# Kernel optimization log

Measured on AMD Instinct MI355X. Metric: run time of the kernel, lower is better.

The kernel has to match this reference:

```python
import jax, jax.numpy as jnp
import numpy as np
from jax import lax

B, T_CAP, V, E, D = 64, 32, 32000, 1024, 1024  # embed_dim == encoder_dim required by the module


def _lstm_cell(x, h, c, W_ih, W_hh, b_ih, b_hh):
    # gates: [B, 4D]; PyTorch LSTMCell gate order: i, f, g, o
    gates = x @ W_ih.T + b_ih + h @ W_hh.T + b_hh
    i, f, g, o = jnp.split(gates, 4, axis=-1)
    c_new = jax.nn.sigmoid(f) * c + jax.nn.sigmoid(i) * jnp.tanh(g)
    h_new = jax.nn.sigmoid(o) * jnp.tanh(c_new)
    return h_new, c_new


def setup_inputs() -> dict:
    key = jax.random.key(0)
    ks = jax.random.split(key, 9)
    encoder_out = jax.random.normal(ks[0], (B, E), jnp.float32)
    encoded_captions = jax.random.randint(ks[1], (B, T_CAP), 0, V, dtype=jnp.int64)
    caption_lengths = jax.random.randint(ks[2], (B, 1), 2, T_CAP + 1, dtype=jnp.int64)
    caption_lengths = caption_lengths.at[0, 0].set(T_CAP)  # ensure max decode len = T_CAP-1 (static)
    s = 1.0 / np.sqrt(D).astype(np.float32)
    embedding = jax.random.normal(ks[3], (V, E), jnp.float32)
    W_ih = jax.random.uniform(ks[4], (4 * D, E), jnp.float32, -s, s)
    W_hh = jax.random.uniform(ks[5], (4 * D, D), jnp.float32, -s, s)
    b_ih = jax.random.uniform(ks[6], (4 * D,), jnp.float32, -s, s)
    b_hh = jax.random.uniform(ks[7], (4 * D,), jnp.float32, -s, s)
    fc_W = jax.random.uniform(ks[8], (V, D), jnp.float32, -0.1, 0.1)  # reset_parameters
    fc_b = jnp.zeros((V,), jnp.float32)
    return {"encoder_out": encoder_out, "encoded_captions": encoded_captions,
            "caption_lengths": caption_lengths, "embedding": embedding,
            "W_ih": W_ih, "W_hh": W_hh, "b_ih": b_ih, "b_hh": b_hh,
            "fc_W": fc_W, "fc_b": fc_b}


def reference(encoder_out, encoded_captions, caption_lengths, embedding,
              W_ih, W_hh, b_ih, b_hh, fc_W, fc_b):
    lengths = caption_lengths[:, 0]
    sort_ind = jnp.argsort(-lengths)  # descending, stable (matches torch sort semantics)
    lengths = lengths[sort_ind]
    enc = encoder_out[sort_ind]                       # [B, E]
    caps = encoded_captions[sort_ind]                 # [B, T]
    emb = embedding[caps]                             # [B, T, E]
    decode_lengths = lengths - 1                      # [B]
    t_dec = emb.shape[1] - 1                          # static = T_CAP - 1

    zeros = jnp.zeros((enc.shape[0], D), enc.dtype)
    h, c = _lstm_cell(enc, zeros, zeros, W_ih, W_hh, b_ih, b_hh)  # warm-up step with encoder_out

    # masked update is equivalent to the torch :batch_size_t slicing because
    # lengths are sorted descending -> the active prefix only shrinks over t.
    masks = jnp.arange(t_dec)[:, None] < decode_lengths[None, :]  # [T-1, B]
    xs = jnp.swapaxes(emb[:, :t_dec], 0, 1)                       # [T-1, B, E]

    def step(carry, inp):
        h, c = carry
        x_t, m = inp
        hn, cn = _lstm_cell(x_t, h, c, W_ih, W_hh, b_ih, b_hh)
        m2 = m[:, None]
        h = jnp.where(m2, hn, h)
        c = jnp.where(m2, cn, c)
        # dropout in eval mode == identity
        preds = (h @ fc_W.T + fc_b) * m2.astype(h.dtype)  # inactive rows stay 0
        return (h, c), preds

    (_, _), preds = lax.scan(step, (h, c), (xs, masks))
    predictions = jnp.swapaxes(preds, 0, 1)  # [B, T-1, V]
    return predictions, decode_lengths, sort_ind
```

## Files before the change

kernel.cpp:

```cpp
#include <hip/hip_runtime.h>
#include <cstddef>
#include <cstdint>

#define PRED_N 63488000

typedef unsigned short u16;
typedef unsigned long long u64;
typedef __attribute__((ext_vector_type(8))) unsigned short us8;
typedef __attribute__((ext_vector_type(4))) float f32x4;
typedef __attribute__((ext_vector_type(8))) __bf16 bf16x8;

__device__ __forceinline__ float bf2f(u16 h){
  unsigned u = ((unsigned)h) << 16;
  return __builtin_bit_cast(float, u);
}
__device__ __forceinline__ u16 f2bf(float f){
  unsigned u = __builtin_bit_cast(unsigned, f);
  u += 0x7FFFu + ((u >> 16) & 1u);
  return (u16)(u >> 16);
}
__device__ __forceinline__ float sigf(float x){ return 1.f/(1.f + __expf(-x)); }
__device__ __forceinline__ float tanhf_(float x){ return 1.f - 2.f/(__expf(2.f*x) + 1.f); }

__device__ __forceinline__ f32x4 mfma16(us8 a, us8 b, f32x4 c){
  return __builtin_amdgcn_mfma_f32_16x16x32_bf16(
      __builtin_bit_cast(bf16x8, a), __builtin_bit_cast(bf16x8, b), c, 0, 0, 0);
}
__device__ __forceinline__ u64 pack4bf(const float* h){
  return (u64)f2bf(h[0]) | ((u64)f2bf(h[1]) << 16)
       | ((u64)f2bf(h[2]) << 32) | ((u64)f2bf(h[3]) << 48);
}
__device__ __forceinline__ us8 pack8(float4 a, float4 b){
  us8 r;
  r[0]=f2bf(a.x); r[1]=f2bf(a.y); r[2]=f2bf(a.z); r[3]=f2bf(a.w);
  r[4]=f2bf(b.x); r[5]=f2bf(b.y); r[6]=f2bf(b.z); r[7]=f2bf(b.w);
  return r;
}
__device__ __forceinline__ float ldf(const void* p, int f32, int i){
  return f32 ? ((const float*)p)[i] : bf2f(((const u16*)p)[i]);
}
__device__ __forceinline__ int ldi(const int* p, int i64, int i){
  return i64 ? p[2*i] : p[i];
}
__device__ __forceinline__ void stH(u16* p, u64 v){
  __hip_atomic_store((u64*)p, v, __ATOMIC_RELAXED, __HIP_MEMORY_SCOPE_AGENT);
}
__device__ __forceinline__ us8 ldH8(const u16* p){
  union { u64 q[2]; us8 v; } u;
  u.q[0] = __hip_atomic_load((const u64*)p,       __ATOMIC_RELAXED, __HIP_MEMORY_SCOPE_AGENT);
  u.q[1] = __hip_atomic_load((const u64*)(p + 4), __ATOMIC_RELAXED, __HIP_MEMORY_SCOPE_AGENT);
  return u.v;
}

__global__ void k_detect(const unsigned* __restrict__ embw, const int* __restrict__ lenw,
                         int* __restrict__ flags){
  if(threadIdx.x == 0){
    int hits = 0;
    for(int i = 0; i < 16; ++i){
      unsigned w = embw[i];
      int elo = (w >> 7) & 0xFF, ehi = (w >> 23) & 0xFF;
      hits += (elo >= 112 && elo <= 133) && (ehi >= 112 && ehi <= 133);
    }
    flags[0] = (hits >= 12) ? 0 : 1;
    int orv = 0;
    for(int i = 0; i < 4; ++i) orv |= lenw[2*i + 1];
    flags[1] = (orv == 0) ? 1 : 0;
    __hip_atomic_store((unsigned*)(flags + 48), 0u, __ATOMIC_RELAXED, __HIP_MEMORY_SCOPE_AGENT);
  }
}

__global__ void k_setup(const int* __restrict__ lens, int* __restrict__ wsI,
                        const int* __restrict__ flags, void* __restrict__ out){
  const int i = threadIdx.x;
  const int f32 = flags[0], i64 = flags[1];
  const int li = ldi(lens, i64, i);
  int rank = 0;
  for(int j = 0; j < 64; ++j){
    const int lj = ldi(lens, i64, j);
    rank += (lj > li) || (lj == li && j < i);
  }
  wsI[rank]      = i;
  wsI[64 + rank] = li - 1;
  if(f32){
    ((float*)out)[PRED_N + rank]      = (float)(li - 1);
    ((float*)out)[PRED_N + 64 + rank] = (float)i;
  } else {
    ((u16*)out)[PRED_N + rank]      = f2bf((float)(li - 1));
    ((u16*)out)[PRED_N + 64 + rank] = f2bf((float)i);
  }
}

__global__ void __launch_bounds__(256) k_conv16(const void* __restrict__ W,
    const int* __restrict__ flags, u16* __restrict__ dst, int n8){
  if(!flags[0]) return;
  const int stride = gridDim.x * 256;
  for(int i = blockIdx.x * 256 + threadIdx.x; i < n8; i += stride){
    const float4* s = (const float4*)W + 2 * (size_t)i;
    ((us8*)dst)[i] = pack8(s[0], s[1]);
  }
}

__global__ void __launch_bounds__(256) k_gather(const void* __restrict__ enc,
    const int* __restrict__ caps, const void* __restrict__ emb,
    const int* __restrict__ wsI, const int* __restrict__ flags, u16* __restrict__ X){
  const int r = blockIdx.x, t = r >> 6, b = r & 63;
  const int f32 = flags[0], i64 = flags[1];
  const int sb = wsI[b];
  const size_t rowoff = (t == 0) ? (size_t)sb * 1024
                                 : (size_t)ldi(caps, i64, sb * 32 + (t - 1)) * 1024;
  const void* base = (t == 0) ? enc : emb;
  u16* dst = X + (size_t)r * 1024;
  if(f32){
    const float4* src = (const float4*)((const float*)base + rowoff);
    float4 v = src[threadIdx.x];
    u64 w = (u64)f2bf(v.x) | ((u64)f2bf(v.y) << 16)
          | ((u64)f2bf(v.z) << 32) | ((u64)f2bf(v.w) << 48);
    ((u64*)dst)[threadIdx.x] = w;
  } else {
    const uint2* src = (const uint2*)((const u16*)base + rowoff);
    ((uint2*)dst)[threadIdx.x] = src[threadIdx.x];
  }
}

__device__ __forceinline__ void gemm_main(const u16* __restrict__ A, const void* __restrict__ Bv,
    int bF32, int arowmax, u16* As, u16* Bs, f32x4 (&acc)[4][4]){
  const int tid = threadIdx.x, wave = tid >> 6, lane = tid & 63;
  const int mq = (wave >> 1) * 64, nq = (wave & 1) * 64;
  const int l15 = lane & 15, lq = lane >> 4;
  const int r0 = lane >> 2, c0 = (lane & 3) * 8;
  const int sww = ((r0 & 7) << 3);
  const int swr = ((l15 & 7) << 3);
  const u16* Bb = (const u16*)Bv; const float* Bf = (const float*)Bv;
  for(int k0 = 0; k0 < 1024; k0 += 32){
    us8 av[2], bv[2];
#pragma unroll
    for(int c2 = 0; c2 < 2; ++c2){
      const int chunk = wave * 2 + c2;
      int ar = chunk * 16 + r0; if(ar > arowmax) ar = arowmax;
      av[c2] = *(const us8*)(A + (size_t)ar * 1024 + k0 + c0);
      const size_t bo = (size_t)(chunk * 16 + r0) * 1024 + k0 + c0;
      if(bF32){
        const float* p = Bf + bo;
        bv[c2] = pack8(*(const float4*)p, *(const float4*)(p + 4));
      } else {
        bv[c2] = *(const us8*)(Bb + bo);
      }
    }
    __syncthreads();
#pragma unroll
    for(int c2 = 0; c2 < 2; ++c2){
      const int chunk = wave * 2 + c2;
      *(us8*)&As[(chunk * 512 + r0 * 32 + c0) ^ sww] = av[c2];
      *(us8*)&Bs[(chunk * 512 + r0 * 32 + c0) ^ sww] = bv[c2];
    }
    __syncthreads();
    us8 af[4], bfv[4];
#pragma unroll
    for(int i = 0; i < 4; ++i){
      af[i]  = *(const us8*)&As[((mq + i * 16 + l15) * 32 + lq * 8) ^ swr];
      bfv[i] = *(const us8*)&Bs[((nq + i * 16 + l15) * 32 + lq * 8) ^ swr];
    }
#pragma unroll
    for(int i = 0; i < 4; ++i)
#pragma unroll
      for(int j = 0; j < 4; ++j)
        acc[i][j] = mfma16(af[i], bfv[j], acc[i][j]);
  }
}

__global__ void __launch_bounds__(256) k_gemm_gates(const u16* __restrict__ X,
    const void* __restrict__ Wih, const u16* __restrict__ Wih16c,
    const void* __restrict__ bih, const void* __restrict__ bhh,
    const int* __restrict__ flags, float* __restrict__ gatesx){
  __shared__ u16 As[4096], Bs[4096];
  const int tid = threadIdx.x, wave = tid >> 6, lane = tid & 63;
  const int bm = blockIdx.x, bn = blockIdx.y;
  const int mq = (wave >> 1) * 64, nq = (wave & 1) * 64;
  const int l15 = lane & 15, lq = lane >> 4;
  const int f32 = flags[0];
  const u16* Wb = f32 ? Wih16c : (const u16*)Wih;
  f32x4 acc[4][4] = {};
  gemm_main(X + (size_t)bm * 128 * 1024, Wb + (size_t)bn * 128 * 1024, 0, 127, As, Bs, acc);
  const int rowb = bm * 128 + mq, colb = bn * 128 + nq;
#pragma unroll
  for(int j = 0; j < 4; ++j){
    const int col = colb + j * 16 + l15;
    const float bias = ldf(bih, f32, col) + ldf(bhh, f32, col);
#pragma unroll
    for(int i = 0; i < 4; ++i)
#pragma unroll
      for(int v = 0; v < 4; ++v){
        const int row = rowb + i * 16 + lq * 4 + v;
        gatesx[(size_t)row * 4096 + col] = acc[i][j][v] + bias;
      }
  }
}

__device__ __forceinline__ void gbar(unsigned* bar, unsigned tgt, int tid){
  __syncthreads();
  if(tid == 0){
    __hip_atomic_fetch_add(bar, 1u, __ATOMIC_RELAXED, __HIP_MEMORY_SCOPE_AGENT);
    while(__hip_atomic_load(bar, __ATOMIC_RELAXED, __HIP_MEMORY_SCOPE_AGENT) < tgt)
      __builtin_amdgcn_s_sleep(2);
  }
  __syncthreads();
  asm volatile("" ::: "memory");
}

__global__ void __launch_bounds__(256, 1) k_rnn5(const void* __restrict__ Whh,
    const u16* __restrict__ Whh16c, const float* __restrict__ gatesx,
    const int* __restrict__ wsI, const int* __restrict__ flags,
    u16* __restrict__ Hbuf, unsigned* __restrict__ bar){
  __shared__ __align__(16) float red[4096];
  __shared__ __align__(16) float hl[256];
  const int tid = threadIdx.x, wave = tid >> 6, lane = tid & 63, blk = blockIdx.x;
  const int l15 = lane & 15, lq = lane >> 4;
  const int m = tid >> 2, dr = tid & 3;
  const int dim = blk * 4 + dr;
  const int dl = wsI[64 + m];
  const u16* W = flags[0] ? Whh16c : (const u16*)Whh;

  float c1, h1;
  {
    const float* gx0 = gatesx + (size_t)m * 4096 + dim;
    const float iv = gx0[0], gv = gx0[2048], ov = gx0[3072];
    c1 = sigf(iv) * tanhf_(gv);
    h1 = sigf(ov) * tanhf_(c1);
  }
  hl[m * 4 + dr] = h1;
  const int brow = (l15 >> 2) * 1024 + blk * 4 + (l15 & 3);
  us8 breg[8];
  {
    const u16* Bp = W + (size_t)brow * 1024 + wave * 256 + lq * 8;
#pragma unroll
    for(int kt = 0; kt < 8; ++kt) breg[kt] = *(const us8*)(Bp + kt * 32);
  }
  __syncthreads();
  if(tid < 64) stH(Hbuf + (size_t)tid * 1024 + blk * 4, pack4bf(&hl[tid * 4]));
  gbar(bar, 256u, tid);

#pragma unroll 1
  for(int t = 0; t < 31; ++t){
    const u16* Ht = Hbuf + (size_t)t * 65536 + wave * 256 + lq * 8;
    us8 af[32];
#pragma unroll
    for(int kt = 0; kt < 8; ++kt)
#pragma unroll
      for(int mi = 0; mi < 4; ++mi)
        af[kt * 4 + mi] = ldH8(Ht + (size_t)(mi * 16 + l15) * 1024 + kt * 32);
    f32x4 acc[4] = {};
#pragma unroll
    for(int kt = 0; kt < 8; ++kt)
#pragma unroll
      for(int mi = 0; mi < 4; ++mi)
        acc[mi] = mfma16(af[kt * 4 + mi], breg[kt], acc[mi]);
#pragma unroll
    for(int mi = 0; mi < 4; ++mi)
#pragma unroll
      for(int v = 0; v < 4; ++v)
        red[wave * 1024 + (mi * 16 + lq * 4 + v) * 16 + l15] = acc[mi][v];
    __syncthreads();
    const float* gx = gatesx + ((size_t)(t + 1) * 64 + m) * 4096 + dim;
    float g4[4];
#pragma unroll
    for(int g = 0; g < 4; ++g){
      const int n = g * 4 + dr;
      g4[g] = red[m * 16 + n] + red[1024 + m * 16 + n]
            + red[2048 + m * 16 + n] + red[3072 + m * 16 + n]
            + gx[(size_t)g * 1024];
    }
    if(t < dl){
      const float cn = sigf(g4[1]) * c1 + sigf(g4[0]) * tanhf_(g4[2]);
      c1 = cn;
      h1 = sigf(g4[3]) * tanhf_(cn);
    }
    hl[m * 4 + dr] = h1;
    __syncthreads();
    if(tid < 64) stH(Hbuf + ((size_t)(t + 1) * 64 + tid) * 1024 + blk * 4, pack4bf(&hl[tid * 4]));
    if(t < 30) gbar(bar, 256u * (t + 2), tid);
  }
}

__global__ void __launch_bounds__(256) k_gemm_fc(const u16* __restrict__ H,
    const void* __restrict__ fcW, const u16* __restrict__ fcW16, const int useW16,
    const void* __restrict__ fcb, const int* __restrict__ declen,
    const int* __restrict__ flags, void* __restrict__ out){
  __shared__ u16 smem[8192];
  u16* As = smem; u16* Bs = smem + 4096;
  const int tid = threadIdx.x, wave = tid >> 6, lane = tid & 63;
  const int bid = blockIdx.x;
  const int L = (bid & 7) * 500 + (bid >> 3);
  const int bm = L & 15, bn = L >> 4;
  const int mq = (wave >> 1) * 64, nq = (wave & 1) * 64;
  const int l15 = lane & 15, lq = lane >> 4;
  const int f32 = flags[0];
  const void* Bbase; int bf32;
  if(f32){
    if(useW16){ Bbase = fcW16 + (size_t)bn * 131072; bf32 = 0; }
    else      { Bbase = (const float*)fcW + (size_t)bn * 131072; bf32 = 1; }
  } else      { Bbase = (const u16*)fcW + (size_t)bn * 131072; bf32 = 0; }
  f32x4 acc[4][4] = {};
  const int amax0 = 1983 - bm * 128;
  gemm_main(H + (size_t)bm * 131072, Bbase, bf32, amax0 > 127 ? 127 : amax0, As, Bs, acc);
  float bias[4];
#pragma unroll
  for(int j = 0; j < 4; ++j) bias[j] = ldf(fcb, f32, bn * 128 + nq + j * 16 + l15);
  __syncthreads();
  for(int i = 0; i < 4; ++i){
#pragma unroll
    for(int v = 0; v < 4; ++v){
      const int row = bm * 128 + mq + i * 16 + lq * 4 + v;
      const int s = (wave >> 1) * 16 + lq * 4 + v;
      bool act = false;
      if(row < 1984) act = ((row >> 6) < declen[row & 63]);
#pragma unroll
      for(int j = 0; j < 4; ++j){
        const float val = act ? (acc[i][j][v] + bias[j]) : 0.f;
        const int cl = nq + j * 16 + l15;
        if(f32) ((float*)smem)[s * 128 + cl] = val;
        else    smem[s * 128 + cl] = f2bf(val);
      }
    }
    __syncthreads();
    if(f32){
#pragma unroll
      for(int p = 0; p < 4; ++p){
        const int idx = p * 256 + tid;
        const int s = idx >> 5, c = (idx & 31) * 4;
        const int grow = bm * 128 + (s >> 4) * 64 + i * 16 + (s & 15);
        if(grow < 1984){
          const int tt = grow >> 6, b = grow & 63;
          *(float4*)((float*)out + (size_t)b * 992000 + (size_t)tt * 32000 + bn * 128 + c)
              = *(const float4*)((const float*)smem + s * 128 + c);
        }
      }
    } else {
#pragma unroll
      for(int p = 0; p < 2; ++p){
        const int idx = p * 256 + tid;
        const int s = idx >> 4, c = (idx & 15) * 8;
        const int grow = bm * 128 + (s >> 4) * 64 + i * 16 + (s & 15);
        if(grow < 1984){
          const int tt = grow >> 6, b = grow & 63;
          *(us8*)((u16*)out + (size_t)b * 992000 + (size_t)tt * 32000 + bn * 128 + c)
              = *(const us8*)(smem + s * 128 + c);
        }
      }
    }
    __syncthreads();
  }
}

extern "C" void kernel_launch(void* const* d_in, const int* in_sizes, int n_in,
                              void* d_out, int out_size, void* d_ws, size_t ws_size,
                              hipStream_t stream){
  const void* enc = d_in[0];
  const int*  caps = (const int*)d_in[1];
  const int*  lens = (const int*)d_in[2];
  const void* emb = d_in[3];
  const void* Wih = d_in[4];
  const void* Whh = d_in[5];
  const void* bih = d_in[6];
  const void* bhh = d_in[7];
  const void* fcW = d_in[8];
  const void* fcb = d_in[9];

  float* gatesx = (float*)d_out;
  u16*   Xbuf   = (u16*)((char*)d_out + (size_t)32*1024*1024);
  u16*   Whh16  = (u16*)((char*)d_out + (size_t)36*1024*1024);
  u16*   Wih16  = (u16*)((char*)d_out + (size_t)36*1024*1024 + 8388608);
  char* ws = (char*)d_ws;
  int*      flags = (int*)ws;
  unsigned* bar   = (unsigned*)(ws + 192);
  int*      wsI   = (int*)(ws + 256);
  u16*      Hbuf  = (u16*)(ws + (size_t)512*1024);
  u16*      fcW16 = (u16*)(ws + (size_t)8*1024*1024);
  const int useFc16 = (ws_size >= (size_t)74*1024*1024) ? 1 : 0;

  hipLaunchKernelGGL(k_detect, dim3(1), dim3(64), 0, stream,
                     (const unsigned*)emb, lens, flags);
  hipLaunchKernelGGL(k_setup, dim3(1), dim3(64), 0, stream, lens, wsI, flags, d_out);
  hipLaunchKernelGGL(k_conv16, dim3(2048), dim3(256), 0, stream, Wih, flags, Wih16, 524288);
  hipLaunchKernelGGL(k_conv16, dim3(2048), dim3(256), 0, stream, Whh, flags, Whh16, 524288);
  if(useFc16)
    hipLaunchKernelGGL(k_conv16, dim3(4096), dim3(256), 0, stream, fcW, flags, fcW16, 4096000);
  hipLaunchKernelGGL(k_gather, dim3(2048), dim3(256), 0, stream, enc, caps, emb, wsI, flags, Xbuf);
  hipLaunchKernelGGL(k_gemm_gates, dim3(16, 32), dim3(256), 0, stream,
                     Xbuf, Wih, Wih16, bih, bhh, flags, gatesx);

  {
    const void* a0 = Whh; const u16* a1 = Whh16; const float* a2 = gatesx;
    const int* a3 = wsI; const int* a4 = flags; u16* a5 = Hbuf; unsigned* a6 = bar;
    void* kargs[] = {(void*)&a0, (void*)&a1, (void*)&a2, (void*)&a3,
                     (void*)&a4, (void*)&a5, (void*)&a6};
    hipLaunchCooperativeKernel((const void*)k_rnn5, dim3(256), dim3(256), kargs, 0, stream);
  }

  hipLaunchKernelGGL(k_gemm_fc, dim3(4000), dim3(256), 0, stream,
                     Hbuf + (size_t)64 * 1024, fcW, fcW16, useFc16, fcb, wsI + 64, flags, d_out);
}
```

Baseline: 1.151 ms.

## Replace atomic-counter grid barrier with per-block flag array barrier and prefetch gates

The grid barrier in the recurrent kernel no longer has every block do an atomic fetch-add on one shared counter. Each block now stores its step number into its own flag slot, and a full wavefront polls all 256 flags with 64-bit loads, using a wave-wide vote to decide when to exit. This is meant to remove contention and serialization on the single counter. The precomputed input-gate values for each step are also loaded at the start of the iteration, so their latency overlaps the recurrent matmul. The trade-off is more polling traffic per block and a workspace region that must be zeroed in the detect kernel.

Measured after the change: 1.123 ms. 2.4% less time.

```diff
diff --git a/kernel.cpp b/kernel.cpp
--- a/kernel.cpp
+++ b/kernel.cpp
@@ -54,7 +54,11 @@
 
 __global__ void k_detect(const unsigned* __restrict__ embw, const int* __restrict__ lenw,
                          int* __restrict__ flags){
-  if(threadIdx.x == 0){
+  const int tid = threadIdx.x;
+  for(int i = tid; i < 256; i += 64)
+    __hip_atomic_store((unsigned*)(flags + 1024) + i, 0u,
+                       __ATOMIC_RELAXED, __HIP_MEMORY_SCOPE_AGENT);
+  if(tid == 0){
     int hits = 0;
     for(int i = 0; i < 16; ++i){
       unsigned w = embw[i];
@@ -65,7 +69,6 @@
     int orv = 0;
     for(int i = 0; i < 4; ++i) orv |= lenw[2*i + 1];
     flags[1] = (orv == 0) ? 1 : 0;
-    __hip_atomic_store((unsigned*)(flags + 48), 0u, __ATOMIC_RELAXED, __HIP_MEMORY_SCOPE_AGENT);
   }
 }
 
@@ -196,21 +199,29 @@
   }
 }
 
-__device__ __forceinline__ void gbar(unsigned* bar, unsigned tgt, int tid){
+__device__ __forceinline__ void gbar(unsigned* flagv, unsigned tgt, int tid, int bid){
   __syncthreads();
-  if(tid == 0){
-    __hip_atomic_fetch_add(bar, 1u, __ATOMIC_RELAXED, __HIP_MEMORY_SCOPE_AGENT);
-    while(__hip_atomic_load(bar, __ATOMIC_RELAXED, __HIP_MEMORY_SCOPE_AGENT) < tgt)
-      __builtin_amdgcn_s_sleep(2);
+  if(tid < 64){
+    if(tid == 0)
+      __hip_atomic_store(flagv + bid, tgt, __ATOMIC_RELAXED, __HIP_MEMORY_SCOPE_AGENT);
+    const u64* fp = (const u64*)flagv + tid * 2;
+    for(;;){
+      const u64 q0 = __hip_atomic_load(fp,     __ATOMIC_RELAXED, __HIP_MEMORY_SCOPE_AGENT);
+      const u64 q1 = __hip_atomic_load(fp + 1, __ATOMIC_RELAXED, __HIP_MEMORY_SCOPE_AGENT);
+      const bool ok = ((unsigned)q0 >= tgt) && ((unsigned)(q0 >> 32) >= tgt)
+                   && ((unsigned)q1 >= tgt) && ((unsigned)(q1 >> 32) >= tgt);
+      if(__all(ok)) break;
+      __builtin_amdgcn_s_sleep(1);
+    }
   }
   __syncthreads();
   asm volatile("" ::: "memory");
 }
 
-__global__ void __launch_bounds__(256, 1) k_rnn5(const void* __restrict__ Whh,
+__global__ void __launch_bounds__(256, 1) k_rnn6(const void* __restrict__ Whh,
     const u16* __restrict__ Whh16c, const float* __restrict__ gatesx,
     const int* __restrict__ wsI, const int* __restrict__ flags,
-    u16* __restrict__ Hbuf, unsigned* __restrict__ bar){
+    u16* __restrict__ Hbuf, unsigned* __restrict__ flagv){
   __shared__ __align__(16) float red[4096];
   __shared__ __align__(16) float hl[256];
   const int tid = threadIdx.x, wave = tid >> 6, lane = tid & 63, blk = blockIdx.x;
@@ -237,10 +248,14 @@
   }
   __syncthreads();
   if(tid < 64) stH(Hbuf + (size_t)tid * 1024 + blk * 4, pack4bf(&hl[tid * 4]));
-  gbar(bar, 256u, tid);
+  gbar(flagv, 1u, tid, blk);
 
 #pragma unroll 1
   for(int t = 0; t < 31; ++t){
+    const float* gx = gatesx + ((size_t)(t + 1) * 64 + m) * 4096 + dim;
+    float gpre[4];
+#pragma unroll
+    for(int g = 0; g < 4; ++g) gpre[g] = gx[(size_t)g * 1024];
     const u16* Ht = Hbuf + (size_t)t * 65536 + wave * 256 + lq * 8;
     us8 af[32];
 #pragma unroll
@@ -260,14 +275,13 @@
       for(int v = 0; v < 4; ++v)
         red[wave * 1024 + (mi * 16 + lq * 4 + v) * 16 + l15] = acc[mi][v];
     __syncthreads();
-    const float* gx = gatesx + ((size_t)(t + 1) * 64 + m) * 4096 + dim;
     float g4[4];
 #pragma unroll
     for(int g = 0; g < 4; ++g){
       const int n = g * 4 + dr;
       g4[g] = red[m * 16 + n] + red[1024 + m * 16 + n]
             + red[2048 + m * 16 + n] + red[3072 + m * 16 + n]
-            + gx[(size_t)g * 1024];
+            + gpre[g];
     }
     if(t < dl){
       const float cn = sigf(g4[1]) * c1 + sigf(g4[0]) * tanhf_(g4[2]);
@@ -277,7 +291,7 @@
     hl[m * 4 + dr] = h1;
     __syncthreads();
     if(tid < 64) stH(Hbuf + ((size_t)(t + 1) * 64 + tid) * 1024 + blk * 4, pack4bf(&hl[tid * 4]));
-    if(t < 30) gbar(bar, 256u * (t + 2), tid);
+    if(t < 30) gbar(flagv, (unsigned)(t + 2), tid, blk);
   }
 }
 
@@ -371,8 +385,8 @@
   u16*   Wih16  = (u16*)((char*)d_out + (size_t)36*1024*1024 + 8388608);
   char* ws = (char*)d_ws;
   int*      flags = (int*)ws;
-  unsigned* bar   = (unsigned*)(ws + 192);
   int*      wsI   = (int*)(ws + 256);
+  unsigned* flagv = (unsigned*)(ws + 4096);
   u16*      Hbuf  = (u16*)(ws + (size_t)512*1024);
   u16*      fcW16 = (u16*)(ws + (size_t)8*1024*1024);
   const int useFc16 = (ws_size >= (size_t)74*1024*1024) ? 1 : 0;
@@ -390,10 +404,10 @@
 
   {
     const void* a0 = Whh; const u16* a1 = Whh16; const float* a2 = gatesx;
-    const int* a3 = wsI; const int* a4 = flags; u16* a5 = Hbuf; unsigned* a6 = bar;
+    const int* a3 = wsI; const int* a4 = flags; u16* a5 = Hbuf; unsigned* a6 = flagv;
     void* kargs[] = {(void*)&a0, (void*)&a1, (void*)&a2, (void*)&a3,
                      (void*)&a4, (void*)&a5, (void*)&a6};
-    hipLaunchCooperativeKernel((const void*)k_rnn5, dim3(256), dim3(256), kargs, 0, stream);
+    hipLaunchCooperativeKernel((const void*)k_rnn6, dim3(256), dim3(256), kargs, 0, stream);
   }
 
   hipLaunchKernelGGL(k_gemm_fc, dim3(4000), dim3(256), 0, stream,
```
